# Kernel tuning notes

Measured on AMD Instinct MI355X. Metric: run time of the kernel, lower is better.

## Reference

```python
import jax, jax.numpy as jnp
import numpy as np
from jax import lax

B, DF, DO, DK, DV, KER, STR = 32, 2048, 2048, 128, 128, 4, 2
STR_Q = int(np.ceil(DF / DO))  # = 1, so query conv has kernel=stride=1


def conv1d(x, w, stride):
    # x: [B, Cin, L], w: [Cout, Cin, K] -> [B, Cout, Lout], VALID, no bias
    return lax.conv_general_dilated(x, w, (stride,), 'VALID',
                                    dimension_numbers=('NCH', 'OIH', 'NCH'))


def layernorm(x, w, b, eps):
    m = jnp.mean(x, axis=-1, keepdims=True)
    v = jnp.mean(jnp.square(x - m), axis=-1, keepdims=True)
    return (x - m) * lax.rsqrt(v + eps) * w + b


def setup_inputs() -> dict:
    key = jax.random.key(0)
    ks = jax.random.split(key, 10)
    s = 0.02
    return {
        'features': jax.random.normal(ks[0], (B, DF), dtype=jnp.float32),
        'shuffled_index': jax.random.randint(ks[1], (DF,), 0, DF, dtype=jnp.int32),
        'ln_w': jnp.ones((DF,), jnp.float32),
        'ln_b': jnp.zeros((DF,), jnp.float32),
        'q_w': jax.random.normal(ks[2], (DK, 1, STR_Q), jnp.float32) * s,
        'k_w': jax.random.normal(ks[3], (DK, 1, KER), jnp.float32) * s,
        'v_w': jax.random.normal(ks[4], (DV, 1, KER), jnp.float32) * s,
        'conv_w': jax.random.normal(ks[5], (1, DV, 1), jnp.float32) * s,
        'bn_ln_w': jnp.ones((DO,), jnp.float32),
        'bn_ln_b': jnp.zeros((DO,), jnp.float32),
        'w1_w': jax.random.normal(ks[6], (DO, DO), jnp.float32) * s,
        'w1_b': jnp.zeros((DO,), jnp.float32),
        'w2_w': jax.random.normal(ks[7], (DO, DO), jnp.float32) * s,
        'w2_b': jnp.zeros((DO,), jnp.float32),
    }


def reference(features, shuffled_index, ln_w, ln_b, q_w, k_w, v_w, conv_w,
              bn_ln_w, bn_ln_b, w1_w, w1_b, w2_w, w2_b):
    residual = features                               # [B, DF]
    q_in = layernorm(features, ln_w, ln_b, 1e-5)[:, None, :]   # [B,1,DF]
    shuf = features[:, shuffled_index][:, None, :]             # [B,1,DF]

    query = conv1d(q_in, q_w, STR_Q)                  # [B, DK, DO]
    key_t = conv1d(shuf, k_w, STR)                    # [B, DK, NC]
    value = conv1d(shuf, v_w, STR)                    # [B, DV, NC]

    # ScaledDotProduction, temperature=1, dropout eval-mode identity
    attn = jnp.einsum('bkq,bkc->bqc', query, key_t)   # [B, DO, NC]
    attn = jax.nn.softmax(attn, axis=2)
    out = jnp.einsum('bqc,bvc->bqv', attn, value)     # [B, DO, DV]

    # output Conv1d(d_v -> 1, kernel 1) applied to [B, DV, DO]
    out = jnp.einsum('bqv,v->bq', out, conv_w[0, :, 0])  # [B, DO]
    out = out + residual                              # d_features == d_out

    # Bottleneck FFN
    r = out
    h = layernorm(out, bn_ln_w, bn_ln_b, 1e-6)
    h = jax.nn.relu(h @ w1_w.T + w1_b) @ w2_w.T + w2_b
    out = h + r
    return (out, attn)
```

## Files before the change

kernel.cpp:

```cpp
#include <hip/hip_runtime.h>
#include <float.h>

#define NB 32
#define D  2048
#define NC 1023

#define OFF_LN   0
#define OFF_SW   (NB*D)
#define OFF_MM   (OFF_SW + 2*NB*NC)
#define OFF_OUT1 (OFF_MM + 2*NB)
#define OFF_LN2  (OFF_OUT1 + NB*D)
#define OFF_H    (OFF_LN2 + NB*D)

__device__ __forceinline__ float wred_sum(float x){
  #pragma unroll
  for (int o = 32; o; o >>= 1) x += __shfl_xor(x, o);
  return x;
}

__global__ __launch_bounds__(256) void prep_kernel(
    const float* __restrict__ feat, const int* __restrict__ idx,
    const float* __restrict__ ln_w, const float* __restrict__ ln_b,
    const float* __restrict__ q_w,  const float* __restrict__ k_w,
    const float* __restrict__ v_w,  const float* __restrict__ conv_w,
    float* __restrict__ ws)
{
  __shared__ float sh_feat[D];
  __shared__ float sh_shuf[D];
  __shared__ float red_s[4][2];
  __shared__ float red_k[4][8];
  __shared__ float red_mm[4][2];

  const int b = blockIdx.x;
  const int t = threadIdx.x;
  const int wid = t >> 6;

  const float4* fb4 = (const float4*)(feat + b * D);
  float4* sf4 = (float4*)sh_feat;
  float4 fv[2];
  float s1 = 0.f, s2 = 0.f;
  #pragma unroll
  for (int j = 0; j < 2; ++j) {
    float4 v = fb4[t + j * 256];
    fv[j] = v;
    sf4[t + j * 256] = v;
    s1 += (v.x + v.y) + (v.z + v.w);
    s2 += fmaf(v.x, v.x, fmaf(v.y, v.y, fmaf(v.z, v.z, v.w * v.w)));
  }

  float pk[4] = {0,0,0,0}, pv[4] = {0,0,0,0};
  if (t < 128) {
    float qv = q_w[t], cv = conv_w[t];
    #pragma unroll
    for (int j = 0; j < 4; ++j) {
      pk[j] = qv * k_w[t * 4 + j];
      pv[j] = cv * v_w[t * 4 + j];
    }
  }
  s1 = wred_sum(s1); s2 = wred_sum(s2);
  #pragma unroll
  for (int j = 0; j < 4; ++j) { pk[j] = wred_sum(pk[j]); pv[j] = wred_sum(pv[j]); }
  if ((t & 63) == 0) {
    red_s[wid][0] = s1; red_s[wid][1] = s2;
    #pragma unroll
    for (int j = 0; j < 4; ++j) { red_k[wid][j] = pk[j]; red_k[wid][4 + j] = pv[j]; }
  }
  __syncthreads();

  const float S1 = red_s[0][0] + red_s[1][0] + red_s[2][0] + red_s[3][0];
  const float S2 = red_s[0][1] + red_s[1][1] + red_s[2][1] + red_s[3][1];
  float kq[4], vw[4];
  #pragma unroll
  for (int j = 0; j < 4; ++j) {
    kq[j] = red_k[0][j] + red_k[1][j] + red_k[2][j] + red_k[3][j];
    vw[j] = red_k[0][4+j] + red_k[1][4+j] + red_k[2][4+j] + red_k[3][4+j];
  }
  const float mean = S1 * (1.f / D);
  const float rstd = rsqrtf(S2 * (1.f / D) - mean * mean + 1e-5f);

  float* lnp = ws + OFF_LN + b * D;
  const float4* lw4 = (const float4*)ln_w;
  const float4* lb4 = (const float4*)ln_b;
  #pragma unroll
  for (int j = 0; j < 2; ++j) {
    int i = t + j * 256;
    float4 v = fv[j], w = lw4[i], bb = lb4[i], o;
    o.x = (v.x - mean) * rstd * w.x + bb.x;
    o.y = (v.y - mean) * rstd * w.y + bb.y;
    o.z = (v.z - mean) * rstd * w.z + bb.z;
    o.w = (v.w - mean) * rstd * w.w + bb.w;
    ((float4*)lnp)[i] = o;
  }

  #pragma unroll
  for (int j = 0; j < 8; ++j) {
    int i = t + j * 256;
    sh_shuf[i] = sh_feat[idx[i]];
  }
  __syncthreads();

  float2* swp = (float2*)(ws + OFF_SW) + b * NC;
  float lmax = -FLT_MAX, lmin = FLT_MAX;
  #pragma unroll
  for (int j = 0; j < 4; ++j) {
    int c = t + j * 256;
    if (c < NC) {
      float a0 = sh_shuf[2*c], a1 = sh_shuf[2*c+1], a2 = sh_shuf[2*c+2], a3 = sh_shuf[2*c+3];
      float sv = fmaf(a0, kq[0], fmaf(a1, kq[1], fmaf(a2, kq[2], a3 * kq[3])));
      float wv = fmaf(a0, vw[0], fmaf(a1, vw[1], fmaf(a2, vw[2], a3 * vw[3])));
      float2 p; p.x = sv; p.y = wv;
      swp[c] = p;
      lmax = fmaxf(lmax, sv);
      lmin = fminf(lmin, sv);
    }
  }
  #pragma unroll
  for (int o = 32; o; o >>= 1) {
    lmax = fmaxf(lmax, __shfl_xor(lmax, o));
    lmin = fminf(lmin, __shfl_xor(lmin, o));
  }
  if ((t & 63) == 0) { red_mm[wid][0] = lmax; red_mm[wid][1] = lmin; }
  __syncthreads();
  if (t == 0) {
    ws[OFF_MM + b]      = fmaxf(fmaxf(red_mm[0][0], red_mm[1][0]), fmaxf(red_mm[2][0], red_mm[3][0]));
    ws[OFF_MM + NB + b] = fminf(fminf(red_mm[0][1], red_mm[1][1]), fminf(red_mm[2][1], red_mm[3][1]));
  }
}

__global__ __launch_bounds__(128) void attn_kernel(
    const float* __restrict__ feat, float* __restrict__ ws,
    float* __restrict__ out)
{
  __shared__ float ebuf[1024];
  __shared__ float sred[4];

  const int row = blockIdx.x;
  const int b = row >> 11;
  const int t = threadIdx.x;

  const float alpha = ws[OFF_LN + row];
  const float smax = ws[OFF_MM + b], smin = ws[OFF_MM + NB + b];
  const float m = (alpha >= 0.f) ? alpha * smax : alpha * smin;
  const float2* sw = (const float2*)(ws + OFF_SW) + b * NC;

  float l = 0.f, acc = 0.f;
  #pragma unroll
  for (int j = 0; j < 8; ++j) {
    int c = t + j * 128;
    if (c < NC) {
      float2 p = sw[c];
      float e = __expf(fmaf(alpha, p.x, -m));
      ebuf[c] = e;
      l += e;
      acc = fmaf(e, p.y, acc);
    }
  }
  #pragma unroll
  for (int o = 32; o; o >>= 1) { l += __shfl_xor(l, o); acc += __shfl_xor(acc, o); }
  const int wid = t >> 6;
  if ((t & 63) == 0) { sred[wid * 2] = l; sred[wid * 2 + 1] = acc; }
  __syncthreads();
  l = sred[0] + sred[2];
  acc = sred[1] + sred[3];
  const float inv = 1.f / l;

  float* ap = out + NB * D + (size_t)row * NC;
  #pragma unroll
  for (int j = 0; j < 8; ++j) {
    int c = t + j * 128;
    if (c < NC) ap[c] = ebuf[c] * inv;
  }
  if (t == 0) ws[OFF_OUT1 + row] = fmaf(acc, inv, feat[row]);
}

__global__ __launch_bounds__(256) void ln2_init_kernel(
    const float* __restrict__ bnw, const float* __restrict__ bnb,
    const float* __restrict__ w1b, const float* __restrict__ w2b,
    float* __restrict__ ws, float* __restrict__ out)
{
  __shared__ float red_s[4][2];
  const int b = blockIdx.x, t = threadIdx.x;
  const int wid = t >> 6;
  const float4* x4 = (const float4*)(ws + OFF_OUT1 + b * D);
  float4 xv[2];
  float s1 = 0.f, s2 = 0.f;
  #pragma unroll
  for (int j = 0; j < 2; ++j) {
    float4 v = x4[t + j * 256];
    xv[j] = v;
    s1 += (v.x + v.y) + (v.z + v.w);
    s2 += fmaf(v.x, v.x, fmaf(v.y, v.y, fmaf(v.z, v.z, v.w * v.w)));
  }
  s1 = wred_sum(s1); s2 = wred_sum(s2);
  if ((t & 63) == 0) { red_s[wid][0] = s1; red_s[wid][1] = s2; }
  __syncthreads();
  const float S1 = red_s[0][0] + red_s[1][0] + red_s[2][0] + red_s[3][0];
  const float S2 = red_s[0][1] + red_s[1][1] + red_s[2][1] + red_s[3][1];
  const float mean = S1 * (1.f / D);
  const float rstd = rsqrtf(S2 * (1.f / D) - mean * mean + 1e-6f);

  float4* ln2p = (float4*)(ws + OFF_LN2 + b * D);
  float4* hp   = (float4*)(ws + OFF_H   + b * D);
  float4* op   = (float4*)out + b * (D / 4);
  const float4* bw4 = (const float4*)bnw;
  const float4* bb4 = (const float4*)bnb;
  const float4* w1b4 = (const float4*)w1b;
  const float4* w2b4 = (const float4*)w2b;
  #pragma unroll
  for (int j = 0; j < 2; ++j) {
    int i = t + j * 256;
    float4 v = xv[j], w = bw4[i], bb = bb4[i], o;
    o.x = (v.x - mean) * rstd * w.x + bb.x;
    o.y = (v.y - mean) * rstd * w.y + bb.y;
    o.z = (v.z - mean) * rstd * w.z + bb.z;
    o.w = (v.w - mean) * rstd * w.w + bb.w;
    ln2p[i] = o;
    hp[i] = w1b4[i];
    float4 w2 = w2b4[i], oo;
    oo.x = v.x + w2.x; oo.y = v.y + w2.y; oo.z = v.z + w2.z; oo.w = v.w + w2.w;
    op[i] = oo;
  }
}

template<int RELU>
__global__ __launch_bounds__(256) void gemm_kernel(
    const float* __restrict__ X, const float* __restrict__ W,
    float* __restrict__ out)
{
  __shared__ float xs[32 * 68];
  __shared__ float wt[32 * 68];
  const int nb = blockIdx.x & 63;
  const int kb = blockIdx.x >> 6;
  const int n0 = nb * 32;
  const int t = threadIdx.x;
  const int row = t >> 3, kl = t & 7;
  const int tr = t >> 4, tc = (t & 15) * 4;

  float acc[32];
  #pragma unroll
  for (int m = 0; m < 32; ++m) acc[m] = 0.f;

  for (int ch = 0; ch < 8; ++ch) {
    const int kc = kb * 512 + ch * 64;
    #pragma unroll
    for (int jj = 0; jj < 2; ++jj) {
      int r = tr + jj * 16;
      float4 v = *(const float4*)(X + r * 2048 + kc + tc);
      if (RELU) {
        v.x = fmaxf(v.x, 0.f); v.y = fmaxf(v.y, 0.f);
        v.z = fmaxf(v.z, 0.f); v.w = fmaxf(v.w, 0.f);
      }
      *(float4*)(xs + r * 68 + tc) = v;
      float4 wv = *(const float4*)(W + (n0 + r) * 2048 + kc + tc);
      *(float4*)(wt + r * 68 + tc) = wv;
    }
    __syncthreads();
    const float4 wa = *(float4*)(wt + row * 68 + kl * 8);
    const float4 wb = *(float4*)(wt + row * 68 + kl * 8 + 4);
    #pragma unroll
    for (int m = 0; m < 32; ++m) {
      float4 xa = *(float4*)(xs + m * 68 + kl * 8);
      float4 xb = *(float4*)(xs + m * 68 + kl * 8 + 4);
      acc[m] = fmaf(xa.x, wa.x, fmaf(xa.y, wa.y, fmaf(xa.z, wa.z, fmaf(xa.w, wa.w,
               fmaf(xb.x, wb.x, fmaf(xb.y, wb.y, fmaf(xb.z, wb.z, fmaf(xb.w, wb.w, acc[m]))))))));
    }
    __syncthreads();
  }
  #pragma unroll
  for (int m = 0; m < 32; ++m) {
    acc[m] += __shfl_xor(acc[m], 1);
    acc[m] += __shfl_xor(acc[m], 2);
    acc[m] += __shfl_xor(acc[m], 4);
  }
  #pragma unroll
  for (int i = 0; i < 4; ++i) {
    int m = kl * 4 + i;
    atomicAdd(out + m * 2048 + n0 + row, acc[m]);
  }
}

extern "C" void kernel_launch(void* const* d_in, const int* in_sizes, int n_in,
                              void* d_out, int out_size, void* d_ws, size_t ws_size,
                              hipStream_t stream)
{
  (void)in_sizes; (void)n_in; (void)out_size; (void)ws_size;
  const float* feat   = (const float*)d_in[0];
  const int*   idx    = (const int*)d_in[1];
  const float* ln_w   = (const float*)d_in[2];
  const float* ln_b   = (const float*)d_in[3];
  const float* q_w    = (const float*)d_in[4];
  const float* k_w    = (const float*)d_in[5];
  const float* v_w    = (const float*)d_in[6];
  const float* conv_w = (const float*)d_in[7];
  const float* bnw    = (const float*)d_in[8];
  const float* bnb    = (const float*)d_in[9];
  const float* w1w    = (const float*)d_in[10];
  const float* w1b    = (const float*)d_in[11];
  const float* w2w    = (const float*)d_in[12];
  const float* w2b    = (const float*)d_in[13];
  float* out = (float*)d_out;
  float* ws  = (float*)d_ws;

  prep_kernel<<<dim3(NB), dim3(256), 0, stream>>>(feat, idx, ln_w, ln_b, q_w, k_w, v_w, conv_w, ws);
  attn_kernel<<<dim3(NB * D), dim3(128), 0, stream>>>(feat, ws, out);
  ln2_init_kernel<<<dim3(NB), dim3(256), 0, stream>>>(bnw, bnb, w1b, w2b, ws, out);
  gemm_kernel<0><<<dim3(256), dim3(256), 0, stream>>>(ws + OFF_LN2, w1w, ws + OFF_H);
  gemm_kernel<1><<<dim3(256), dim3(256), 0, stream>>>(ws + OFF_H, w2w, out);
}
```

Baseline: 414.5 us.

## Batch attention rows per block with contiguous vector nontemporal stores; double GEMM split-K

```diff
diff --git a/kernel.cpp b/kernel.cpp
--- a/kernel.cpp
+++ b/kernel.cpp
@@ -4,6 +4,9 @@
 #define NB 32
 #define D  2048
 #define NC 1023
+#define RPB 8
+
+typedef float f32x4 __attribute__((ext_vector_type(4)));
 
 #define OFF_LN   0
 #define OFF_SW   (NB*D)
@@ -127,50 +130,63 @@
   }
 }
 
-__global__ __launch_bounds__(128) void attn_kernel(
+__global__ __launch_bounds__(256) void attn_kernel(
     const float* __restrict__ feat, float* __restrict__ ws,
     float* __restrict__ out)
 {
-  __shared__ float ebuf[1024];
-  __shared__ float sred[4];
-
-  const int row = blockIdx.x;
-  const int b = row >> 11;
+  __shared__ float ebuf[RPB * 1024];
+  __shared__ float sinv[RPB];
+
+  const int row0 = blockIdx.x * RPB;
+  const int b = row0 >> 11;
   const int t = threadIdx.x;
-
-  const float alpha = ws[OFF_LN + row];
+  const int wid = t >> 6, lane = t & 63;
+
   const float smax = ws[OFF_MM + b], smin = ws[OFF_MM + NB + b];
-  const float m = (alpha >= 0.f) ? alpha * smax : alpha * smin;
   const float2* sw = (const float2*)(ws + OFF_SW) + b * NC;
 
-  float l = 0.f, acc = 0.f;
+  #pragma unroll
+  for (int rr = 0; rr < 2; ++rr) {
+    const int r = wid * 2 + rr;
+    const int row = row0 + r;
+    const float alpha = ws[OFF_LN + row];
+    const float m = (alpha >= 0.f) ? alpha * smax : alpha * smin;
+    float* eb = ebuf + r * NC;
+    float l = 0.f, acc = 0.f;
+    #pragma unroll
+    for (int j = 0; j < 16; ++j) {
+      int c = lane + j * 64;
+      if (c < NC) {
+        float2 p = sw[c];
+        float e = __expf(fmaf(alpha, p.x, -m));
+        eb[c] = e;
+        l += e;
+        acc = fmaf(e, p.y, acc);
+      }
+    }
+    #pragma unroll
+    for (int o = 32; o; o >>= 1) { l += __shfl_xor(l, o); acc += __shfl_xor(acc, o); }
+    if (lane == 0) {
+      float inv = 1.f / l;
+      sinv[r] = inv;
+      ws[OFF_OUT1 + row] = fmaf(acc, inv, feat[row]);
+    }
+  }
+  __syncthreads();
+
+  f32x4* base = (f32x4*)(out + NB * D + (size_t)row0 * NC);
+  const f32x4* eb4 = (const f32x4*)ebuf;
   #pragma unroll
   for (int j = 0; j < 8; ++j) {
-    int c = t + j * 128;
-    if (c < NC) {
-      float2 p = sw[c];
-      float e = __expf(fmaf(alpha, p.x, -m));
-      ebuf[c] = e;
-      l += e;
-      acc = fmaf(e, p.y, acc);
-    }
-  }
-  #pragma unroll
-  for (int o = 32; o; o >>= 1) { l += __shfl_xor(l, o); acc += __shfl_xor(acc, o); }
-  const int wid = t >> 6;
-  if ((t & 63) == 0) { sred[wid * 2] = l; sred[wid * 2 + 1] = acc; }
-  __syncthreads();
-  l = sred[0] + sred[2];
-  acc = sred[1] + sred[3];
-  const float inv = 1.f / l;
-
-  float* ap = out + NB * D + (size_t)row * NC;
-  #pragma unroll
-  for (int j = 0; j < 8; ++j) {
-    int c = t + j * 128;
-    if (c < NC) ap[c] = ebuf[c] * inv;
-  }
-  if (t == 0) ws[OFF_OUT1 + row] = fmaf(acc, inv, feat[row]);
+    int i4 = t + j * 256;
+    if (i4 < 2046) {
+      f32x4 v = eb4[i4];
+      int g = i4 * 4;
+      int r0 = g / NC, r1 = (g + 1) / NC, r2 = (g + 2) / NC, r3 = (g + 3) / NC;
+      v.x *= sinv[r0]; v.y *= sinv[r1]; v.z *= sinv[r2]; v.w *= sinv[r3];
+      __builtin_nontemporal_store(v, base + i4);
+    }
+  }
 }
 
 __global__ __launch_bounds__(256) void ln2_init_kernel(
@@ -240,8 +256,8 @@
   #pragma unroll
   for (int m = 0; m < 32; ++m) acc[m] = 0.f;
 
-  for (int ch = 0; ch < 8; ++ch) {
-    const int kc = kb * 512 + ch * 64;
+  for (int ch = 0; ch < 4; ++ch) {
+    const int kc = kb * 256 + ch * 64;
     #pragma unroll
     for (int jj = 0; jj < 2; ++jj) {
       int r = tr + jj * 16;
@@ -302,8 +318,8 @@
   float* ws  = (float*)d_ws;
 
   prep_kernel<<<dim3(NB), dim3(256), 0, stream>>>(feat, idx, ln_w, ln_b, q_w, k_w, v_w, conv_w, ws);
-  attn_kernel<<<dim3(NB * D), dim3(128), 0, stream>>>(feat, ws, out);
+  attn_kernel<<<dim3(NB * D / RPB), dim3(256), 0, stream>>>(feat, ws, out);
   ln2_init_kernel<<<dim3(NB), dim3(256), 0, stream>>>(bnw, bnb, w1b, w2b, ws, out);
-  gemm_kernel<0><<<dim3(256), dim3(256), 0, stream>>>(ws + OFF_LN2, w1w, ws + OFF_H);
-  gemm_kernel<1><<<dim3(256), dim3(256), 0, stream>>>(ws + OFF_H, w2w, out);
-}
+  gemm_kernel<0><<<dim3(512), dim3(256), 0, stream>>>(ws + OFF_LN2, w1w, ws + OFF_H);
+  gemm_kernel<1><<<dim3(512), dim3(256), 0, stream>>>(ws + OFF_H, w2w, out);
+}
```

Result: faster. 354.3 us (-14.5%).
